# Kernel optimization log

Measured on AMD Instinct MI355X. Metric: run time of the kernel, lower is better.

Reference implementation:

```python
import jax, jax.numpy as jnp
import numpy as np

B = 2048          # number of drug pairs (graphs)
N_PER_DRUG = 32   # nodes per drug subgraph (uniform for static shapes)
F = 128           # node_feature_dim
H = 128           # hidden_dim
E = 1048576       # total edges (~avg degree 8 per node)


def setup_inputs() -> dict:
    key = jax.random.key(0)
    ks = jax.random.split(key, 12)
    total = B * 2 * N_PER_DRUG
    x = jax.random.normal(ks[0], (total, F), dtype=jnp.float32)
    # edges generated within each drug subgraph (2B blocks of N_PER_DRUG nodes)
    blk = jax.random.randint(ks[1], (E,), 0, 2 * B)
    src = blk * N_PER_DRUG + jax.random.randint(ks[2], (E,), 0, N_PER_DRUG)
    dst = blk * N_PER_DRUG + jax.random.randint(ks[3], (E,), 0, N_PER_DRUG)
    edge_index = jnp.stack([src, dst]).astype(jnp.int32)
    ptr = (jnp.arange(B + 1) * 2 * N_PER_DRUG).astype(jnp.int32)
    split = jnp.full((B,), N_PER_DRUG, dtype=jnp.int32)

    def lin(k, shape, fan_in):
        return jax.random.normal(k, shape, dtype=jnp.float32) * (1.0 / np.sqrt(fan_in))

    return {
        "x": x, "edge_index": edge_index, "ptr": ptr, "split": split,
        "W1": lin(ks[4], (F, H), F), "b1": jnp.zeros((H,), jnp.float32),
        "W2": lin(ks[5], (H, H), H), "b2": jnp.zeros((H,), jnp.float32),
        "Wm1": lin(ks[6], (2 * H, H), 2 * H), "bm1": jnp.zeros((H,), jnp.float32),
        "Wm2": lin(ks[7], (H, 1), H), "bm2": jnp.zeros((1,), jnp.float32),
    }


def reference(x, edge_index, ptr, split, W1, b1, W2, b2, Wm1, bm1, Wm2, bm2):
    num_nodes = x.shape[0]
    nB = ptr.shape[0] - 1
    idx = jnp.arange(num_nodes, dtype=jnp.int32)
    g = (jnp.searchsorted(ptr, idx, side="right") - 1).astype(jnp.int32)
    local = idx - ptr[g]
    drug = (local >= split[g]).astype(jnp.int32)
    seg = 2 * g + drug                      # (graph, drug-half) segment id
    src, dst = edge_index[0], edge_index[1]
    # edge valid iff same graph AND same drug half (== the per-sample masks)
    w = (seg[src] == seg[dst]).astype(x.dtype)
    # GCN normalization with self-loops (shared by both layers)
    deg = jax.ops.segment_sum(w, dst, num_segments=num_nodes) + 1.0
    dinv = jax.lax.rsqrt(deg)
    norm = dinv[src] * dinv[dst] * w        # [E]
    self_norm = (dinv * dinv)[:, None]      # [N,1]

    def gcn(h, W, b):
        hw = h @ W
        agg = jax.ops.segment_sum(norm[:, None] * hw[src], dst, num_segments=num_nodes)
        return agg + self_norm * hw + b

    h = jax.nn.relu(gcn(x, W1, b1))
    h = jax.nn.relu(gcn(h, W2, b2))
    nseg = 2 * nB
    cnt = jax.ops.segment_sum(jnp.ones((num_nodes,), x.dtype), seg, num_segments=nseg)
    pooled = jax.ops.segment_sum(h, seg, num_segments=nseg) / jnp.maximum(cnt, 1.0)[:, None]
    pair = jnp.concatenate([pooled[0::2], pooled[1::2]], axis=1)  # [B, 2H]
    z = jax.nn.relu(pair @ Wm1 + bm1) @ Wm2 + bm2
    return jax.nn.sigmoid(z).reshape(-1)
```

## Files before the change

kernel.cpp:

```cpp
#include <hip/hip_runtime.h>
#include <hip/hip_bf16.h>
#include <math.h>

#define NF 128
#define ECAP 512

typedef short bf16x8 __attribute__((ext_vector_type(8)));
typedef float f32x4  __attribute__((ext_vector_type(4)));

union U8 { unsigned u[4]; bf16x8 v; };

__device__ __forceinline__ unsigned pk2(float lo, float hi) {
    union { __hip_bfloat162 h2; unsigned u; } c;
    c.h2 = __float22bfloat162_rn(make_float2(lo, hi));
    return c.u;
}
__device__ __forceinline__ unsigned short f2bf(float f) {
    union { __hip_bfloat16 h; unsigned short u; } c;
    c.h = __float2bfloat16(f);
    return c.u;
}

__global__ void k_segtab(const int* __restrict__ ptr, const int* __restrict__ split,
                         int nseg, int* __restrict__ segstart, int* __restrict__ segcnt) {
    int s = blockIdx.x * blockDim.x + threadIdx.x;
    if (s >= nseg) return;
    int g = s >> 1;
    int base = ptr[g];
    int sp = split[g];
    segstart[s] = (s & 1) ? base + sp : base;
    segcnt[s]   = (s & 1) ? (ptr[g + 1] - base - sp) : sp;
}

__global__ void k_node(const int* __restrict__ ptr, const int* __restrict__ split,
                       int nB, int N, unsigned* __restrict__ segloc) {
    int i = blockIdx.x * blockDim.x + threadIdx.x;
    if (i >= N) return;
    int lo = 0, hi = nB + 1;
    while (lo < hi) { int mid = (lo + hi) >> 1; if (ptr[mid] <= i) lo = mid + 1; else hi = mid; }
    int g = lo - 1;
    int local = i - ptr[g];
    int sp = split[g];
    int drug = (local >= sp) ? 1 : 0;
    int seg = 2 * g + drug;
    int loc = local - (drug ? sp : 0);
    segloc[i] = ((unsigned)seg << 8) | (unsigned)loc;
}

__global__ void __launch_bounds__(1024) k_sort(
    const int* __restrict__ src, const int* __restrict__ dst, int E, int epb, int nseg,
    const unsigned* __restrict__ segloc, int* __restrict__ cursor,
    unsigned short* __restrict__ ebuf)
{
    __shared__ unsigned cnt[4096];
    __shared__ unsigned gbase[4096];
    const int t  = threadIdx.x;
    const int e0 = blockIdx.x * epb;
    const int e1 = (e0 + epb < E) ? e0 + epb : E;

    for (int i = t; i < 4096; i += 1024) cnt[i] = 0;
    __syncthreads();

    for (int e = e0 + t; e < e1; e += 1024) {
        unsigned ss = segloc[src[e]], dd = segloc[dst[e]];
        if ((ss >> 8) == (dd >> 8)) atomicAdd(&cnt[ss >> 8], 1u);
    }
    __syncthreads();

    for (int i = t; i < nseg; i += 1024) {
        unsigned c = cnt[i];
        if (c) gbase[i] = (unsigned)atomicAdd(&cursor[i], (int)c);
    }
    __syncthreads();
    for (int i = t; i < 4096; i += 1024) cnt[i] = 0;
    __syncthreads();

    for (int e = e0 + t; e < e1; e += 1024) {
        unsigned ss = segloc[src[e]], dd = segloc[dst[e]];
        unsigned seg = ss >> 8;
        if (seg == (dd >> 8)) {
            unsigned pos = gbase[seg] + atomicAdd(&cnt[seg], 1u);
            if (pos < ECAP)
                ebuf[(seg << 9) + pos] = (unsigned short)(((dd & 63u) << 6) | (ss & 63u));
        }
    }
}

__global__ void k_wt(const float* __restrict__ W1, const float* __restrict__ W2,
                     short* __restrict__ Wt1, short* __restrict__ Wt2) {
    int n = blockIdx.x, k = threadIdx.x;
    Wt1[n * 128 + k] = (short)f2bf(W1[k * 128 + n]);
    Wt2[n * 128 + k] = (short)f2bf(W2[k * 128 + n]);
}

__global__ void __launch_bounds__(64, 2) k_gcn3(
    const float* __restrict__ x,
    const int* __restrict__ segstart, const int* __restrict__ segcnt,
    const int* __restrict__ ecnt, const unsigned short* __restrict__ ebuf,
    const short* __restrict__ Wt1, const float* __restrict__ b1,
    const short* __restrict__ Wt2, const float* __restrict__ b2,
    float* __restrict__ pooled)
{
    __shared__ short xt[128 * 40];
    __shared__ float zbF[2048];
    short* zb = (short*)zbF;

    const int seg = blockIdx.x;
    const int l  = threadIdx.x;
    const int fr = l & 15;
    const int g  = l >> 4;
    const int swz = (fr & 7) << 3;

    const int start = segstart[seg];
    const int cnt   = segcnt[seg];

    const int f0 = (l & 7) * 16;
    const int c0 = (l >> 3) * 4;
    float xr[4][16];
    #pragma unroll
    for (int i = 0; i < 4; ++i) {
        if (c0 + i < cnt) {
            const float4* rp = (const float4*)(x + (size_t)(start + c0 + i) * NF + f0);
            float4 a = rp[0], b = rp[1], c = rp[2], d = rp[3];
            xr[i][0]=a.x; xr[i][1]=a.y; xr[i][2]=a.z; xr[i][3]=a.w;
            xr[i][4]=b.x; xr[i][5]=b.y; xr[i][6]=b.z; xr[i][7]=b.w;
            xr[i][8]=c.x; xr[i][9]=c.y; xr[i][10]=c.z; xr[i][11]=c.w;
            xr[i][12]=d.x; xr[i][13]=d.y; xr[i][14]=d.z; xr[i][15]=d.w;
        } else {
            #pragma unroll
            for (int j = 0; j < 16; ++j) xr[i][j] = 0.f;
        }
    }

    for (int i = l; i < 1088; i += 64) zbF[i] = 0.f;
    __syncthreads();

    {
        int en = ecnt[seg];
        en = en < ECAP ? en : ECAP;
        const unsigned short* eb = ebuf + ((size_t)seg << 9);
        for (int i = l; i < en; i += 64) {
            unsigned c = eb[i];
            if ((c & ((32u << 6) | 32u)) == 0u) {
                atomicAdd(&zbF[((c >> 6) & 31) * 33 + (c & 31)], 1.0f);
            }
        }
    }
    __syncthreads();

    #pragma unroll
    for (int j = 0; j < 16; ++j) {
        uint2 w;
        w.x = pk2(xr[0][j], xr[1][j]);
        w.y = pk2(xr[2][j], xr[3][j]);
        *reinterpret_cast<uint2*>(&xt[(f0 + j) * 40 + c0]) = w;
    }

    {
        int r = l & 31, half = l >> 5;
        float s = 0.f;
        const float* row = &zbF[r * 33 + half * 16];
        #pragma unroll
        for (int k = 0; k < 16; ++k) s += row[k];
        s += __shfl_xor(s, 32);
        float dv = rsqrtf(1.0f + s);
        if (l < 32) zbF[1056 + r] = dv;
    }
    __syncthreads();

    bf16x8 bfr0, bfr1;
    {
        float dr0 = zbF[1056 + fr];
        float dr1 = zbF[1056 + 16 + fr];
        float e0[8], e1[8];
        #pragma unroll
        for (int j = 0; j < 8; ++j) {
            int c = g * 8 + j;
            float dc = zbF[1056 + c];
            float v0 = zbF[fr * 33 + c]        * dr0 * dc;
            float v1 = zbF[(16 + fr) * 33 + c] * dr1 * dc;
            if (fr == c)      v0 += dr0 * dr0;
            if (16 + fr == c) v1 += dr1 * dr1;
            e0[j] = v0; e1[j] = v1;
        }
        U8 u0, u1;
        u0.u[0] = pk2(e0[0], e0[1]); u0.u[1] = pk2(e0[2], e0[3]);
        u0.u[2] = pk2(e0[4], e0[5]); u0.u[3] = pk2(e0[6], e0[7]);
        u1.u[0] = pk2(e1[0], e1[1]); u1.u[1] = pk2(e1[2], e1[3]);
        u1.u[2] = pk2(e1[4], e1[5]); u1.u[3] = pk2(e1[6], e1[7]);
        bfr0 = u0.v; bfr1 = u1.v;
    }
    __syncthreads();

    for (int layer = 0; layer < 2; ++layer) {
        const short* Wt = layer ? Wt2 : Wt1;
        const float* bb = layer ? b2  : b1;

        #pragma unroll
        for (int mt = 0; mt < 8; ++mt) {
            bf16x8 af = *(const bf16x8*)&xt[(mt * 16 + fr) * 40 + g * 8];
            f32x4 z0 = {0.f, 0.f, 0.f, 0.f};
            f32x4 z1 = {0.f, 0.f, 0.f, 0.f};
            z0 = __builtin_amdgcn_mfma_f32_16x16x32_bf16(af, bfr0, z0, 0, 0, 0);
            z1 = __builtin_amdgcn_mfma_f32_16x16x32_bf16(af, bfr1, z1, 0, 0, 0);
            int fb = mt * 16 + 4 * g;
            uint2 w0, w1;
            w0.x = pk2(z0[0], z0[1]); w0.y = pk2(z0[2], z0[3]);
            w1.x = pk2(z1[0], z1[1]); w1.y = pk2(z1[2], z1[3]);
            *reinterpret_cast<uint2*>(&zb[fr * 128 + (fb ^ swz)])        = w0;
            *reinterpret_cast<uint2*>(&zb[(16 + fr) * 128 + (fb ^ swz)]) = w1;
        }
        __syncthreads();

        f32x4 acc[2][8];
        #pragma unroll
        for (int i = 0; i < 2; ++i)
            #pragma unroll
            for (int j = 0; j < 8; ++j) acc[i][j] = (f32x4){0.f, 0.f, 0.f, 0.f};
        #pragma unroll
        for (int kk = 0; kk < 4; ++kk) {
            int ko = kk * 32 + g * 8;
            bf16x8 a0 = *(const bf16x8*)&zb[fr * 128 + (ko ^ swz)];
            bf16x8 a1 = *(const bf16x8*)&zb[(16 + fr) * 128 + (ko ^ swz)];
            #pragma unroll
            for (int nt = 0; nt < 8; ++nt) {
                bf16x8 wf = *(const bf16x8*)&Wt[(nt * 16 + fr) * 128 + ko];
                acc[0][nt] = __builtin_amdgcn_mfma_f32_16x16x32_bf16(a0, wf, acc[0][nt], 0, 0, 0);
                acc[1][nt] = __builtin_amdgcn_mfma_f32_16x16x32_bf16(a1, wf, acc[1][nt], 0, 0, 0);
            }
        }
        __syncthreads();

        if (layer == 0) {
            #pragma unroll
            for (int nt = 0; nt < 8; ++nt) {
                float bv = bb[nt * 16 + fr];
                #pragma unroll
                for (int mt = 0; mt < 2; ++mt) {
                    float h0 = acc[mt][nt][0] + bv; h0 = h0 > 0.f ? h0 : 0.f;
                    float h1 = acc[mt][nt][1] + bv; h1 = h1 > 0.f ? h1 : 0.f;
                    float h2 = acc[mt][nt][2] + bv; h2 = h2 > 0.f ? h2 : 0.f;
                    float h3 = acc[mt][nt][3] + bv; h3 = h3 > 0.f ? h3 : 0.f;
                    uint2 w;
                    w.x = pk2(h0, h1); w.y = pk2(h2, h3);
                    *reinterpret_cast<uint2*>(&xt[(nt * 16 + fr) * 40 + mt * 16 + 4 * g]) = w;
                }
            }
        } else {
            float rcpc = 1.0f / (float)(cnt > 0 ? cnt : 1);
            #pragma unroll
            for (int nt = 0; nt < 8; ++nt) {
                float bv = bb[nt * 16 + fr];
                float pm = 0.f;
                #pragma unroll
                for (int mt = 0; mt < 2; ++mt)
                    #pragma unroll
                    for (int r = 0; r < 4; ++r) {
                        int node = mt * 16 + 4 * g + r;
                        float h = acc[mt][nt][r] + bv;
                        h = h > 0.f ? h : 0.f;
                        if (node < cnt) pm += h;
                    }
                pm += __shfl_xor(pm, 16);
                pm += __shfl_xor(pm, 32);
                if (l < 16) pooled[(size_t)seg * NF + nt * 16 + l] = pm * rcpc;
            }
        }
        __syncthreads();
    }
}

__global__ void __launch_bounds__(128) k_mlp(
    const float* __restrict__ pooled, const float* __restrict__ Wm1,
    const float* __restrict__ bm1, const float* __restrict__ Wm2,
    const float* __restrict__ bm2, float* __restrict__ out) {
    __shared__ float pr[256];
    __shared__ float partial[2];
    int b = blockIdx.x, t = threadIdx.x;
    pr[t]       = pooled[(size_t)(2 * b) * 128 + t];
    pr[128 + t] = pooled[(size_t)(2 * b + 1) * 128 + t];
    __syncthreads();
    float acc = bm1[t];
    #pragma unroll 4
    for (int k = 0; k < 256; ++k) acc += pr[k] * Wm1[k * 128 + t];
    float h = acc > 0.f ? acc : 0.f;
    float v = h * Wm2[t];
    #pragma unroll
    for (int o = 32; o > 0; o >>= 1) v += __shfl_xor(v, o);
    if ((t & 63) == 0) partial[t >> 6] = v;
    __syncthreads();
    if (t == 0) {
        float z = partial[0] + partial[1] + bm2[0];
        out[b] = 1.f / (1.f + expf(-z));
    }
}

static inline size_t alup(size_t v) { return (v + 255) & ~(size_t)255; }

extern "C" void kernel_launch(void* const* d_in, const int* in_sizes, int n_in,
                              void* d_out, int out_size, void* d_ws, size_t ws_size,
                              hipStream_t stream) {
    const float* x     = (const float*)d_in[0];
    const int*   edge  = (const int*)d_in[1];
    const int*   ptr   = (const int*)d_in[2];
    const int*   split = (const int*)d_in[3];
    const float* W1  = (const float*)d_in[4];
    const float* b1  = (const float*)d_in[5];
    const float* W2  = (const float*)d_in[6];
    const float* b2  = (const float*)d_in[7];
    const float* Wm1 = (const float*)d_in[8];
    const float* bm1 = (const float*)d_in[9];
    const float* Wm2 = (const float*)d_in[10];
    const float* bm2 = (const float*)d_in[11];
    float* out = (float*)d_out;

    const int N    = in_sizes[0] / NF;
    const int E    = in_sizes[1] / 2;
    const int nB   = in_sizes[2] - 1;
    const int nseg = 2 * nB;

    char* ws = (char*)d_ws;
    size_t off = 0;
    unsigned*       segloc   = (unsigned*)(ws + off);       off += alup((size_t)N * 4);
    int*            segstart = (int*)(ws + off);            off += alup((size_t)nseg * 4);
    int*            segcnt   = (int*)(ws + off);            off += alup((size_t)nseg * 4);
    int*            cursor   = (int*)(ws + off);            off += alup((size_t)nseg * 4);
    unsigned short* ebuf     = (unsigned short*)(ws + off); off += alup((size_t)nseg * ECAP * 2);
    float*          pooled   = (float*)(ws + off);          off += alup((size_t)nseg * NF * 4);
    short*          Wt1      = (short*)(ws + off);          off += alup(128 * 128 * 2);
    short*          Wt2      = (short*)(ws + off);          off += alup(128 * 128 * 2);

    const int* srcp = edge;
    const int* dstp = edge + E;

    const int NBLK = 64;
    const int epb  = (E + NBLK - 1) / NBLK;

    hipMemsetAsync(cursor, 0, (size_t)nseg * 4, stream);
    k_segtab<<<(nseg + 255) / 256, 256, 0, stream>>>(ptr, split, nseg, segstart, segcnt);
    k_node<<<(N + 255) / 256, 256, 0, stream>>>(ptr, split, nB, N, segloc);
    k_sort<<<NBLK, 1024, 0, stream>>>(srcp, dstp, E, epb, nseg, segloc, cursor, ebuf);
    k_wt<<<128, 128, 0, stream>>>(W1, W2, Wt1, Wt2);
    k_gcn3<<<nseg, 64, 0, stream>>>(x, segstart, segcnt, cursor, ebuf,
                                    Wt1, b1, Wt2, b2, pooled);
    k_mlp<<<nB, 128, 0, stream>>>(pooled, Wm1, bm1, Wm2, bm2, out);
}
```

Before: 246.1 us.

## Fuse prep kernels, widen edge sort grid, shrink GCN LDS, batch MLP pairs

Merges the segment table, node mapping, cursor memset and weight transpose into one prep kernel, which cuts launches. The edge sort now uses many more blocks of 4096 edges each and caches the packed edge codes in registers, so the second pass does not re-read the edge and segloc arrays. The GCN kernel aliases its adjacency scratch onto the xt buffer to reduce LDS and raises occupancy to 3 blocks per CU, with s_setprio around the MFMA sections. The MLP kernel processes 4 pairs per block so each Wm1 load is reused. The tradeoffs are more global cursor atomics from the larger sort grid and extra barriers in the GCN kernel.

```diff
diff --git a/kernel.cpp b/kernel.cpp
--- a/kernel.cpp
+++ b/kernel.cpp
@@ -21,49 +21,68 @@
     return c.u;
 }
 
-__global__ void k_segtab(const int* __restrict__ ptr, const int* __restrict__ split,
-                         int nseg, int* __restrict__ segstart, int* __restrict__ segcnt) {
-    int s = blockIdx.x * blockDim.x + threadIdx.x;
-    if (s >= nseg) return;
-    int g = s >> 1;
-    int base = ptr[g];
-    int sp = split[g];
-    segstart[s] = (s & 1) ? base + sp : base;
-    segcnt[s]   = (s & 1) ? (ptr[g + 1] - base - sp) : sp;
-}
-
-__global__ void k_node(const int* __restrict__ ptr, const int* __restrict__ split,
-                       int nB, int N, unsigned* __restrict__ segloc) {
+__global__ void k_prep(const int* __restrict__ ptr, const int* __restrict__ split,
+                       int nB, int N, int nseg,
+                       unsigned* __restrict__ segloc, int* __restrict__ segstart,
+                       int* __restrict__ segcnt, int* __restrict__ cursor,
+                       const float* __restrict__ W1, const float* __restrict__ W2,
+                       short* __restrict__ Wt1, short* __restrict__ Wt2) {
     int i = blockIdx.x * blockDim.x + threadIdx.x;
-    if (i >= N) return;
-    int lo = 0, hi = nB + 1;
-    while (lo < hi) { int mid = (lo + hi) >> 1; if (ptr[mid] <= i) lo = mid + 1; else hi = mid; }
-    int g = lo - 1;
-    int local = i - ptr[g];
-    int sp = split[g];
-    int drug = (local >= sp) ? 1 : 0;
-    int seg = 2 * g + drug;
-    int loc = local - (drug ? sp : 0);
-    segloc[i] = ((unsigned)seg << 8) | (unsigned)loc;
+    if (i < N) {
+        int lo = 0, hi = nB + 1;
+        while (lo < hi) { int mid = (lo + hi) >> 1; if (ptr[mid] <= i) lo = mid + 1; else hi = mid; }
+        int g = lo - 1;
+        int local = i - ptr[g];
+        int sp = split[g];
+        int drug = (local >= sp) ? 1 : 0;
+        int seg = 2 * g + drug;
+        int loc = local - (drug ? sp : 0);
+        segloc[i] = ((unsigned)seg << 8) | (unsigned)loc;
+    }
+    if (i < nseg) {
+        int g = i >> 1;
+        int base = ptr[g];
+        int sp = split[g];
+        segstart[i] = (i & 1) ? base + sp : base;
+        segcnt[i]   = (i & 1) ? (ptr[g + 1] - base - sp) : sp;
+        cursor[i]   = 0;
+    }
+    if (i < 32768) {
+        int m = i >> 14;
+        int rem = i & 16383;
+        int n = rem & 127;
+        int k = rem >> 7;
+        const float* W = m ? W2 : W1;
+        short* Wt = m ? Wt2 : Wt1;
+        Wt[n * 128 + k] = (short)f2bf(W[k * 128 + n]);
+    }
 }
 
 __global__ void __launch_bounds__(1024) k_sort(
-    const int* __restrict__ src, const int* __restrict__ dst, int E, int epb, int nseg,
+    const int* __restrict__ src, const int* __restrict__ dst, int E, int nseg,
     const unsigned* __restrict__ segloc, int* __restrict__ cursor,
     unsigned short* __restrict__ ebuf)
 {
     __shared__ unsigned cnt[4096];
     __shared__ unsigned gbase[4096];
     const int t  = threadIdx.x;
-    const int e0 = blockIdx.x * epb;
-    const int e1 = (e0 + epb < E) ? e0 + epb : E;
+    const int e0 = blockIdx.x * 4096;
 
     for (int i = t; i < 4096; i += 1024) cnt[i] = 0;
     __syncthreads();
 
-    for (int e = e0 + t; e < e1; e += 1024) {
-        unsigned ss = segloc[src[e]], dd = segloc[dst[e]];
-        if ((ss >> 8) == (dd >> 8)) atomicAdd(&cnt[ss >> 8], 1u);
+    unsigned code[4];
+    #pragma unroll
+    for (int k = 0; k < 4; ++k) {
+        int e = e0 + k * 1024 + t;
+        code[k] = 0xFFFFFFFFu;
+        if (e < E) {
+            unsigned ss = segloc[src[e]], dd = segloc[dst[e]];
+            if ((ss >> 8) == (dd >> 8)) {
+                code[k] = ((ss >> 8) << 12) | ((dd & 63u) << 6) | (ss & 63u);
+                atomicAdd(&cnt[ss >> 8], 1u);
+            }
+        }
     }
     __syncthreads();
 
@@ -75,25 +94,18 @@
     for (int i = t; i < 4096; i += 1024) cnt[i] = 0;
     __syncthreads();
 
-    for (int e = e0 + t; e < e1; e += 1024) {
-        unsigned ss = segloc[src[e]], dd = segloc[dst[e]];
-        unsigned seg = ss >> 8;
-        if (seg == (dd >> 8)) {
-            unsigned pos = gbase[seg] + atomicAdd(&cnt[seg], 1u);
+    #pragma unroll
+    for (int k = 0; k < 4; ++k) {
+        if (code[k] != 0xFFFFFFFFu) {
+            unsigned s = code[k] >> 12;
+            unsigned pos = gbase[s] + atomicAdd(&cnt[s], 1u);
             if (pos < ECAP)
-                ebuf[(seg << 9) + pos] = (unsigned short)(((dd & 63u) << 6) | (ss & 63u));
-        }
-    }
-}
-
-__global__ void k_wt(const float* __restrict__ W1, const float* __restrict__ W2,
-                     short* __restrict__ Wt1, short* __restrict__ Wt2) {
-    int n = blockIdx.x, k = threadIdx.x;
-    Wt1[n * 128 + k] = (short)f2bf(W1[k * 128 + n]);
-    Wt2[n * 128 + k] = (short)f2bf(W2[k * 128 + n]);
-}
-
-__global__ void __launch_bounds__(64, 2) k_gcn3(
+                ebuf[(s << 9) + pos] = (unsigned short)(code[k] & 0xFFFu);
+        }
+    }
+}
+
+__global__ void __launch_bounds__(64, 3) k_gcn5(
     const float* __restrict__ x,
     const int* __restrict__ segstart, const int* __restrict__ segcnt,
     const int* __restrict__ ecnt, const unsigned short* __restrict__ ebuf,
@@ -102,8 +114,8 @@
     float* __restrict__ pooled)
 {
     __shared__ short xt[128 * 40];
-    __shared__ float zbF[2048];
-    short* zb = (short*)zbF;
+    float* Afp = (float*)xt;
+    short* zb  = xt;
 
     const int seg = blockIdx.x;
     const int l  = threadIdx.x;
@@ -132,7 +144,7 @@
         }
     }
 
-    for (int i = l; i < 1088; i += 64) zbF[i] = 0.f;
+    for (int i = l; i < 1088; i += 64) Afp[i] = 0.f;
     __syncthreads();
 
     {
@@ -141,44 +153,35 @@
         const unsigned short* eb = ebuf + ((size_t)seg << 9);
         for (int i = l; i < en; i += 64) {
             unsigned c = eb[i];
-            if ((c & ((32u << 6) | 32u)) == 0u) {
-                atomicAdd(&zbF[((c >> 6) & 31) * 33 + (c & 31)], 1.0f);
-            }
-        }
-    }
-    __syncthreads();
-
-    #pragma unroll
-    for (int j = 0; j < 16; ++j) {
-        uint2 w;
-        w.x = pk2(xr[0][j], xr[1][j]);
-        w.y = pk2(xr[2][j], xr[3][j]);
-        *reinterpret_cast<uint2*>(&xt[(f0 + j) * 40 + c0]) = w;
-    }
+            if ((c & ((32u << 6) | 32u)) == 0u)
+                atomicAdd(&Afp[((c >> 6) & 31) * 33 + (c & 31)], 1.0f);
+        }
+    }
+    __syncthreads();
 
     {
         int r = l & 31, half = l >> 5;
         float s = 0.f;
-        const float* row = &zbF[r * 33 + half * 16];
+        const float* row = &Afp[r * 33 + half * 16];
         #pragma unroll
         for (int k = 0; k < 16; ++k) s += row[k];
         s += __shfl_xor(s, 32);
         float dv = rsqrtf(1.0f + s);
-        if (l < 32) zbF[1056 + r] = dv;
+        if (l < 32) Afp[1056 + r] = dv;
     }
     __syncthreads();
 
     bf16x8 bfr0, bfr1;
     {
-        float dr0 = zbF[1056 + fr];
-        float dr1 = zbF[1056 + 16 + fr];
+        float dr0 = Afp[1056 + fr];
+        float dr1 = Afp[1056 + 16 + fr];
         float e0[8], e1[8];
         #pragma unroll
         for (int j = 0; j < 8; ++j) {
             int c = g * 8 + j;
-            float dc = zbF[1056 + c];
-            float v0 = zbF[fr * 33 + c]        * dr0 * dc;
-            float v1 = zbF[(16 + fr) * 33 + c] * dr1 * dc;
+            float dc = Afp[1056 + c];
+            float v0 = Afp[fr * 33 + c]        * dr0 * dc;
+            float v1 = Afp[(16 + fr) * 33 + c] * dr1 * dc;
             if (fr == c)      v0 += dr0 * dr0;
             if (16 + fr == c) v1 += dr1 * dr1;
             e0[j] = v0; e1[j] = v1;
@@ -192,10 +195,21 @@
     }
     __syncthreads();
 
+    #pragma unroll
+    for (int j = 0; j < 16; ++j) {
+        uint2 w;
+        w.x = pk2(xr[0][j], xr[1][j]);
+        w.y = pk2(xr[2][j], xr[3][j]);
+        *reinterpret_cast<uint2*>(&xt[(f0 + j) * 40 + c0]) = w;
+    }
+    __syncthreads();
+
     for (int layer = 0; layer < 2; ++layer) {
         const short* Wt = layer ? Wt2 : Wt1;
         const float* bb = layer ? b2  : b1;
 
+        unsigned zp[8][4];
+        __builtin_amdgcn_s_setprio(1);
         #pragma unroll
         for (int mt = 0; mt < 8; ++mt) {
             bf16x8 af = *(const bf16x8*)&xt[(mt * 16 + fr) * 40 + g * 8];
@@ -203,10 +217,18 @@
             f32x4 z1 = {0.f, 0.f, 0.f, 0.f};
             z0 = __builtin_amdgcn_mfma_f32_16x16x32_bf16(af, bfr0, z0, 0, 0, 0);
             z1 = __builtin_amdgcn_mfma_f32_16x16x32_bf16(af, bfr1, z1, 0, 0, 0);
+            zp[mt][0] = pk2(z0[0], z0[1]); zp[mt][1] = pk2(z0[2], z0[3]);
+            zp[mt][2] = pk2(z1[0], z1[1]); zp[mt][3] = pk2(z1[2], z1[3]);
+        }
+        __builtin_amdgcn_s_setprio(0);
+        __syncthreads();
+
+        #pragma unroll
+        for (int mt = 0; mt < 8; ++mt) {
             int fb = mt * 16 + 4 * g;
             uint2 w0, w1;
-            w0.x = pk2(z0[0], z0[1]); w0.y = pk2(z0[2], z0[3]);
-            w1.x = pk2(z1[0], z1[1]); w1.y = pk2(z1[2], z1[3]);
+            w0.x = zp[mt][0]; w0.y = zp[mt][1];
+            w1.x = zp[mt][2]; w1.y = zp[mt][3];
             *reinterpret_cast<uint2*>(&zb[fr * 128 + (fb ^ swz)])        = w0;
             *reinterpret_cast<uint2*>(&zb[(16 + fr) * 128 + (fb ^ swz)]) = w1;
         }
@@ -219,19 +241,21 @@
             for (int j = 0; j < 8; ++j) acc[i][j] = (f32x4){0.f, 0.f, 0.f, 0.f};
         #pragma unroll
         for (int kk = 0; kk < 4; ++kk) {
-            int ko = kk * 32 + g * 8;
+            const int ko = kk * 32 + g * 8;
             bf16x8 a0 = *(const bf16x8*)&zb[fr * 128 + (ko ^ swz)];
             bf16x8 a1 = *(const bf16x8*)&zb[(16 + fr) * 128 + (ko ^ swz)];
+            __builtin_amdgcn_s_setprio(1);
             #pragma unroll
             for (int nt = 0; nt < 8; ++nt) {
                 bf16x8 wf = *(const bf16x8*)&Wt[(nt * 16 + fr) * 128 + ko];
                 acc[0][nt] = __builtin_amdgcn_mfma_f32_16x16x32_bf16(a0, wf, acc[0][nt], 0, 0, 0);
                 acc[1][nt] = __builtin_amdgcn_mfma_f32_16x16x32_bf16(a1, wf, acc[1][nt], 0, 0, 0);
             }
-        }
-        __syncthreads();
+            __builtin_amdgcn_s_setprio(0);
+        }
 
         if (layer == 0) {
+            __syncthreads();
             #pragma unroll
             for (int nt = 0; nt < 8; ++nt) {
                 float bv = bb[nt * 16 + fr];
@@ -246,6 +270,7 @@
                     *reinterpret_cast<uint2*>(&xt[(nt * 16 + fr) * 40 + mt * 16 + 4 * g]) = w;
                 }
             }
+            __syncthreads();
         } else {
             float rcpc = 1.0f / (float)(cnt > 0 ? cnt : 1);
             #pragma unroll
@@ -266,32 +291,53 @@
                 if (l < 16) pooled[(size_t)seg * NF + nt * 16 + l] = pm * rcpc;
             }
         }
-        __syncthreads();
     }
 }
 
 __global__ void __launch_bounds__(128) k_mlp(
     const float* __restrict__ pooled, const float* __restrict__ Wm1,
     const float* __restrict__ bm1, const float* __restrict__ Wm2,
-    const float* __restrict__ bm2, float* __restrict__ out) {
-    __shared__ float pr[256];
-    __shared__ float partial[2];
-    int b = blockIdx.x, t = threadIdx.x;
-    pr[t]       = pooled[(size_t)(2 * b) * 128 + t];
-    pr[128 + t] = pooled[(size_t)(2 * b + 1) * 128 + t];
-    __syncthreads();
-    float acc = bm1[t];
+    const float* __restrict__ bm2, float* __restrict__ out, int nB) {
+    __shared__ float pr[4][256];
+    __shared__ float red[4][2];
+    const int b0 = blockIdx.x * 4;
+    const int t = threadIdx.x;
+
+    for (int i = t; i < 1024; i += 128) {
+        int p = i >> 8, c = i & 255;
+        int pair = b0 + p;
+        pr[p][c] = (pair < nB) ? pooled[(size_t)(2 * pair + (c >> 7)) * 128 + (c & 127)] : 0.f;
+    }
+    __syncthreads();
+
+    float acc0 = bm1[t], acc1 = acc0, acc2 = acc0, acc3 = acc0;
     #pragma unroll 4
-    for (int k = 0; k < 256; ++k) acc += pr[k] * Wm1[k * 128 + t];
-    float h = acc > 0.f ? acc : 0.f;
-    float v = h * Wm2[t];
-    #pragma unroll
-    for (int o = 32; o > 0; o >>= 1) v += __shfl_xor(v, o);
-    if ((t & 63) == 0) partial[t >> 6] = v;
-    __syncthreads();
-    if (t == 0) {
-        float z = partial[0] + partial[1] + bm2[0];
-        out[b] = 1.f / (1.f + expf(-z));
+    for (int k = 0; k < 256; ++k) {
+        float w = Wm1[k * 128 + t];
+        acc0 += pr[0][k] * w;
+        acc1 += pr[1][k] * w;
+        acc2 += pr[2][k] * w;
+        acc3 += pr[3][k] * w;
+    }
+    float wm2 = Wm2[t];
+    float v[4];
+    v[0] = (acc0 > 0.f ? acc0 : 0.f) * wm2;
+    v[1] = (acc1 > 0.f ? acc1 : 0.f) * wm2;
+    v[2] = (acc2 > 0.f ? acc2 : 0.f) * wm2;
+    v[3] = (acc3 > 0.f ? acc3 : 0.f) * wm2;
+    #pragma unroll
+    for (int p = 0; p < 4; ++p) {
+        #pragma unroll
+        for (int o = 32; o > 0; o >>= 1) v[p] += __shfl_xor(v[p], o);
+    }
+    if ((t & 63) == 0) {
+        int w = t >> 6;
+        red[0][w] = v[0]; red[1][w] = v[1]; red[2][w] = v[2]; red[3][w] = v[3];
+    }
+    __syncthreads();
+    if (t < 4 && b0 + t < nB) {
+        float z = red[t][0] + red[t][1] + bm2[0];
+        out[b0 + t] = 1.f / (1.f + expf(-z));
     }
 }
 
@@ -333,15 +379,14 @@
     const int* srcp = edge;
     const int* dstp = edge + E;
 
-    const int NBLK = 64;
-    const int epb  = (E + NBLK - 1) / NBLK;
-
-    hipMemsetAsync(cursor, 0, (size_t)nseg * 4, stream);
-    k_segtab<<<(nseg + 255) / 256, 256, 0, stream>>>(ptr, split, nseg, segstart, segcnt);
-    k_node<<<(N + 255) / 256, 256, 0, stream>>>(ptr, split, nB, N, segloc);
-    k_sort<<<NBLK, 1024, 0, stream>>>(srcp, dstp, E, epb, nseg, segloc, cursor, ebuf);
-    k_wt<<<128, 128, 0, stream>>>(W1, W2, Wt1, Wt2);
-    k_gcn3<<<nseg, 64, 0, stream>>>(x, segstart, segcnt, cursor, ebuf,
+    int prepN = N > 32768 ? N : 32768;
+    if (prepN < nseg) prepN = nseg;
+
+    k_prep<<<(prepN + 255) / 256, 256, 0, stream>>>(ptr, split, nB, N, nseg,
+                                                    segloc, segstart, segcnt, cursor,
+                                                    W1, W2, Wt1, Wt2);
+    k_sort<<<(E + 4095) / 4096, 1024, 0, stream>>>(srcp, dstp, E, nseg, segloc, cursor, ebuf);
+    k_gcn5<<<nseg, 64, 0, stream>>>(x, segstart, segcnt, cursor, ebuf,
                                     Wt1, b1, Wt2, b2, pooled);
-    k_mlp<<<nB, 128, 0, stream>>>(pooled, Wm1, bm1, Wm2, bm2, out);
-}
+    k_mlp<<<(nB + 3) / 4, 128, 0, stream>>>(pooled, Wm1, bm1, Wm2, bm2, out, nB);
+}
```

After: 222.1 us. 1.11x faster.
